# Kernel optimization log

Hardware: AMD Instinct MI355X
Metric: run time of the kernel (lower is better)

## Reference

```python
import jax, jax.numpy as jnp
import numpy as np
from jax import lax

B, C, H, W = 64, 64, 56, 56
E, TOPK = 8, 2
DN = ('NCHW', 'OIHW', 'NCHW')


def setup_inputs() -> dict:
    key = jax.random.key(0)
    ks = jax.random.split(key, 9)
    s = 0.05
    return {
        'x': jax.random.normal(ks[0], (B, C, H, W), jnp.float32),
        'gate_w': jax.random.normal(ks[1], (E, C), jnp.float32) * s,
        'gate_b': jnp.zeros((E,), jnp.float32),
        'conv1_w': jax.random.normal(ks[2], (E, C, C, 3, 3), jnp.float32) * s,
        'bn1_s': jnp.ones((E, C), jnp.float32),
        'bn1_b': jnp.zeros((E, C), jnp.float32),
        'conv2_w': jax.random.normal(ks[3], (E, C, C, 3, 3), jnp.float32) * s,
        'bn2_s': jnp.ones((E, C), jnp.float32),
        'bn2_b': jnp.zeros((E, C), jnp.float32),
    }


def _conv3x3(x, w):
    return lax.conv_general_dilated(x, w, (1, 1), ((1, 1), (1, 1)), dimension_numbers=DN)


def _bn(y, scale, bias):
    # eval-mode BatchNorm with running_mean=0, running_var=1 -> per-channel affine
    return y * scale[None, :, None, None] + bias[None, :, None, None]


def _basic_block(x, w1, s1, b1, w2, s2, b2):
    # standard ResNet BasicBlock, stride=1, identity downsample
    out = jax.nn.relu(_bn(_conv3x3(x, w1), s1, b1))
    out = _bn(_conv3x3(out, w2), s2, b2)
    return jax.nn.relu(out + x)


def reference(x, gate_w, gate_b, conv1_w, bn1_s, bn1_b, conv2_w, bn2_s, bn2_b):
    # gate: global average pool over HW -> linear -> top-k softmax weights [B, E]
    pooled = jnp.mean(x, axis=(2, 3))                       # [B, C]
    logits = pooled @ gate_w.T + gate_b                      # [B, E]
    top_vals, top_idx = lax.top_k(logits, TOPK)              # [B, K]
    top_w = jax.nn.softmax(top_vals, axis=-1)                # [B, K]
    dense_w = jnp.zeros((x.shape[0], E), x.dtype).at[
        jnp.arange(x.shape[0])[:, None], top_idx].set(top_w)  # [B, E]

    # run all experts (dense reference for the sparse dispatch/combine)
    ex_out = jax.vmap(lambda w1, s1, b1, w2, s2, b2: _basic_block(x, w1, s1, b1, w2, s2, b2))(
        conv1_w, bn1_s, bn1_b, conv2_w, bn2_s, bn2_b)        # [E, B, C, H, W]
    out = jnp.einsum('be,ebchw->bchw', dense_w, ex_out)
    return out, dense_w
```

## Files before the change

### kernel.cpp

```cpp
#include <hip/hip_runtime.h>


#define BATCH 64
#define CH    64
#define HW_   3136
#define IMG_  (CH*HW_)
#define PLANE (HW_*16)
#define NE    8
#define JOBS  128
#define PWSZ  36864
#define NTILE 13
#define BD    6
#define CGRID (NTILE*2*BATCH)

typedef unsigned short u16;
typedef __attribute__((ext_vector_type(8))) short short8_t;
typedef __attribute__((ext_vector_type(16))) float floatx16;

__device__ u16   g_xb[(size_t)BATCH*IMG_ + 4*PLANE];
__device__ u16   g_h[(size_t)JOBS*IMG_ + 4*PLANE];
__device__ u16   g_pw1[NE * PWSZ];
__device__ u16   g_pw2[NE * PWSZ];
__device__ int   g_eid[JOBS];
__device__ float g_wgt[JOBS];
__device__ float g_pool[49 * BATCH * CH];

__device__ __forceinline__ u16 f2b(float f) {
    unsigned v; __builtin_memcpy(&v, &f, 4);
    return (u16)((v + 0x7FFFu + ((v >> 16) & 1u)) >> 16);
}

__global__ __launch_bounds__(256) void prep_kernel(
    const float* __restrict__ x,
    const float* __restrict__ w1, const float* __restrict__ s1,
    const float* __restrict__ w2, const float* __restrict__ s2)
{
    int bid = blockIdx.x;
    int tid = threadIdx.x;
    if (bid < 2304) {
        int idx = bid * 256 + tid;
        int conv = idx / 294912;
        int i2 = idx - conv * 294912;
        int e = i2 / PWSZ;   int r = i2 - e * PWSZ;
        int s36 = r >> 10;   int r2 = r & 1023;
        int mt  = r2 >> 9;   int r3 = r2 & 511;
        int h   = r3 >> 8;   int r4 = r3 & 255;
        int m   = r4 >> 3;   int j  = r4 & 7;
        int tap = s36 >> 2;
        int ci  = ((s36 & 3) << 4) | (h << 3) | j;
        int M   = mt*32 + m;
        const float* w  = conv ? w2 : w1;
        const float* sc = conv ? s2 : s1;
        float v = w[((e*64 + M)*64 + ci)*9 + tap] * sc[e*64 + M];
        (conv ? g_pw2 : g_pw1)[i2] = f2b(v);
        return;
    }
    __shared__ u16 T[64*66];
    int xid = bid - 2304;
    int b = xid / 49;
    int tile = xid - b*49;
    int pos0 = tile * 64;
    int pin = tid & 63;
    int c0 = tid >> 6;
    const float* xb = x + (size_t)b*IMG_ + pos0 + pin;
    #pragma unroll
    for (int i = 0; i < 16; i++) {
        int ch = c0*16 + i;
        T[pin*66 + ch] = f2b(xb[ch*HW_]);
    }
    __syncthreads();
    u16* ob = g_xb + (size_t)b*IMG_ + (size_t)pos0*16;
    #pragma unroll
    for (int i = 0; i < 16; i++) {
        int j = tid + i*256;
        int kq  = j >> 10;
        int pos = (j >> 4) & 63;
        int c16 = j & 15;
        ob[(size_t)kq*PLANE + pos*16 + c16] = T[pos*66 + kq*16 + c16];
    }
    if (tid < 64) {
        float s = 0.f;
        const float* xc = x + (size_t)b*IMG_ + tid*HW_ + pos0;
        #pragma unroll 4
        for (int p = 0; p < 64; p++) s += xc[p];
        g_pool[tile*(BATCH*CH) + b*64 + tid] = s;
    }
}

__global__ __launch_bounds__(64) void gate_fin_kernel(
    const float* __restrict__ gw, const float* __restrict__ gb,
    float* __restrict__ dw_out)
{
    __shared__ float pooled[CH];
    __shared__ float logits[NE];
    int b = blockIdx.x, t = threadIdx.x;
    float s = 0.f;
    #pragma unroll
    for (int i = 0; i < 49; i++) s += g_pool[i*(BATCH*CH) + b*64 + t];
    pooled[t] = s * (1.f/3136.f);
    __syncthreads();
    if (t < NE) {
        float l = gb[t];
        for (int c = 0; c < CH; c++) l += pooled[c] * gw[t*CH + c];
        logits[t] = l;
    }
    __syncthreads();
    if (t == 0) {
        int i1 = 0; float v1 = logits[0];
        for (int e = 1; e < NE; e++) if (logits[e] > v1) { v1 = logits[e]; i1 = e; }
        int i2 = -1; float v2 = -3.4e38f;
        for (int e = 0; e < NE; e++) if (e != i1 && logits[e] > v2) { v2 = logits[e]; i2 = e; }
        float eb = __expf(v2 - v1);
        float wa = 1.f / (1.f + eb), wb = eb / (1.f + eb);
        for (int e = 0; e < NE; e++) dw_out[b*NE + e] = 0.f;
        dw_out[b*NE + i1] = wa;
        dw_out[b*NE + i2] = wb;
        g_eid[2*b] = i1; g_eid[2*b+1] = i2;
        g_wgt[2*b] = wa; g_wgt[2*b+1] = wb;
    }
}

__device__ __forceinline__ void stageA(
    u16* AL, const u16* __restrict__ pw0, const u16* __restrict__ pw1,
    int mt, int tid)
{
    short8_t st[9];
    #pragma unroll
    for (int i = 0; i < 9; i++) {
        int u = i*512 + tid;
        int es = u >= 2304;
        int r = u - (es ? 2304 : 0);
        int s36 = r >> 6;
        int c = r & 63;
        st[i] = *(const short8_t*)((es ? pw1 : pw0) + s36*1024 + mt*512 + c*8);
    }
    #pragma unroll
    for (int i = 0; i < 9; i++) {
        int u = i*512 + tid;
        int es = u >= 2304;
        int r = u - (es ? 2304 : 0);
        int s36 = r >> 6;
        int c = r & 63;
        *(short8_t*)(AL + (s36*2 + es)*512 + c*8) = st[i];
    }
}

__device__ __forceinline__ void mkOffs(
    unsigned* off, int gn, int y, int xc, int h, unsigned zoff)
{
    #pragma unroll
    for (int tap = 0; tap < 9; tap++) {
        int dy = tap/3 - 1, dx = tap - (tap/3)*3 - 1;
        int p = gn + dy*56 + dx;
        bool vld = ((unsigned)(y + dy) < 56u) && ((unsigned)(xc + dx) < 56u);
        off[tap] = vld ? (unsigned)(p*32 + h*16) : zoff;
    }
}
#define LOADB(base, off, kq) (*(const short8_t*)((base) + (off) + (unsigned)((kq)*PLANE*2)))

__global__ __launch_bounds__(512, 4) void conv1_kernel(const float* __restrict__ b1)
{
    __shared__ u16 AL[36864];
    int wg = blockIdx.x;
    int L  = (wg & 7) * (CGRID/8) + (wg >> 3);
    int b  = L / 26;
    int r  = L - b*26;
    int tile = r >> 1;
    int mt   = r & 1;
    int e0 = g_eid[2*b], e1 = g_eid[2*b+1];
    int tid = threadIdx.x;
    int lane = tid & 63, w = tid >> 6;
    int es = w & 1, pg = w >> 1;
    int l31 = lane & 31, h = lane >> 5;
    int gn0 = tile*256 + pg*64 + l31;
    int gn1 = gn0 + 32;
    int y0 = gn0/56, xc0 = gn0 - y0*56;
    int y1 = gn1/56, xc1 = gn1 - y1*56;
    int e = es ? e1 : e0;
    const char* base = (const char*)(g_xb + (size_t)b*IMG_);
    unsigned zoff = (unsigned)((size_t)(BATCH - b)*IMG_*2);
    const u16* pw0 = g_pw1 + e0*PWSZ;
    const u16* pw1 = g_pw1 + e1*PWSZ;
    int aOff = es*512 + h*256 + l31*8;

    unsigned off0[9], off1[9];
    mkOffs(off0, gn0, y0, xc0, h, zoff);
    mkOffs(off1, gn1, y1, xc1, h, zoff);

    floatx16 accA = {}, accB = {};
    short8_t B0[BD], B1[BD];
    #pragma unroll
    for (int s = 0; s < BD; s++) {
        B0[s] = LOADB(base, off0[s >> 2], s & 3);
        B1[s] = LOADB(base, off1[s >> 2], s & 3);
    }
    stageA(AL, pw0, pw1, mt, tid);
    __syncthreads();

    short8_t Ar[3];
    #pragma unroll
    for (int i = 0; i < 3; i++)
        Ar[i] = *(const short8_t*)(AL + i*1024 + aOff);

    #pragma unroll
    for (int s = 0; s < 36; s++) {
        short8_t bb0 = B0[s % BD];
        short8_t bb1 = B1[s % BD];
        int sp = s + BD;
        if (sp < 36) {
            B0[s % BD] = LOADB(base, off0[sp >> 2], sp & 3);
            B1[s % BD] = LOADB(base, off1[sp >> 2], sp & 3);
        }
        short8_t a = Ar[s % 3];
        if (s + 3 < 36)
            Ar[s % 3] = *(const short8_t*)(AL + (s+3)*1024 + aOff);
        accA = __builtin_amdgcn_mfma_f32_32x32x16_bf16(a, bb0, accA, 0, 0, 0);
        accB = __builtin_amdgcn_mfma_f32_32x32x16_bf16(a, bb1, accB, 0, 0, 0);
    }

    u16* hb = g_h + (size_t)(2*b + es)*IMG_;
    #pragma unroll
    for (int f = 0; f < 2; f++) {
        int gn = f ? gn1 : gn0;
        if (gn < HW_) {
            #pragma unroll
            for (int rg = 0; rg < 4; rg++) {
                union { u16 u[4]; uint2 v; } t;
                #pragma unroll
                for (int rr = 0; rr < 4; rr++) {
                    int m = rg*8 + h*4 + rr;
                    float v = (f ? accB : accA)[rg*4 + rr] + b1[e*64 + mt*32 + m];
                    t.u[rr] = f2b(fmaxf(v, 0.f));
                }
                int kq = mt*2 + (rg >> 1);
                *(uint2*)(hb + (size_t)kq*PLANE + (size_t)gn*16 + (rg & 1)*8 + h*4) = t.v;
            }
        }
    }
}

__global__ __launch_bounds__(512, 4) void conv2_kernel(
    const float* __restrict__ x, const float* __restrict__ b2,
    float* __restrict__ out)
{
    __shared__ u16 AL[36864];
    int wg = blockIdx.x;
    int L  = (wg & 7) * (CGRID/8) + (wg >> 3);
    int b  = L / 26;
    int r  = L - b*26;
    int tile = (NTILE-1) - (r >> 1);
    int mt   = r & 1;
    int e0 = g_eid[2*b], e1 = g_eid[2*b+1];
    int tid = threadIdx.x;
    int lane = tid & 63, w = tid >> 6;
    int es = w & 1, pg = w >> 1;
    int l31 = lane & 31, h = lane >> 5;
    int gn0 = tile*256 + pg*64 + l31;
    int gn1 = gn0 + 32;
    int y0 = gn0/56, xc0 = gn0 - y0*56;
    int y1 = gn1/56, xc1 = gn1 - y1*56;
    int e = es ? e1 : e0;
    float wgt = g_wgt[2*b + es];
    const char* base = (const char*)(g_h + (size_t)(2*b + es)*IMG_);
    unsigned zoff = (unsigned)((size_t)(JOBS - (2*b + es))*IMG_*2);
    const u16* pw0 = g_pw2 + e0*PWSZ;
    const u16* pw1 = g_pw2 + e1*PWSZ;
    int aOff = es*512 + h*256 + l31*8;

    unsigned off0[9], off1[9];
    mkOffs(off0, gn0, y0, xc0, h, zoff);
    mkOffs(off1, gn1, y1, xc1, h, zoff);

    floatx16 accA = {}, accB = {};
    short8_t B0[BD], B1[BD];
    #pragma unroll
    for (int s = 0; s < BD; s++) {
        B0[s] = LOADB(base, off0[s >> 2], s & 3);
        B1[s] = LOADB(base, off1[s >> 2], s & 3);
    }
    stageA(AL, pw0, pw1, mt, tid);
    __syncthreads();

    short8_t Ar[3];
    #pragma unroll
    for (int i = 0; i < 3; i++)
        Ar[i] = *(const short8_t*)(AL + i*1024 + aOff);

    #pragma unroll
    for (int s = 0; s < 36; s++) {
        short8_t bb0 = B0[s % BD];
        short8_t bb1 = B1[s % BD];
        int sp = s + BD;
        if (sp < 36) {
            B0[s % BD] = LOADB(base, off0[sp >> 2], sp & 3);
            B1[s % BD] = LOADB(base, off1[sp >> 2], sp & 3);
        }
        short8_t a = Ar[s % 3];
        if (s + 3 < 36)
            Ar[s % 3] = *(const short8_t*)(AL + (s+3)*1024 + aOff);
        accA = __builtin_amdgcn_mfma_f32_32x32x16_bf16(a, bb0, accA, 0, 0, 0);
        accB = __builtin_amdgcn_mfma_f32_32x32x16_bf16(a, bb1, accB, 0, 0, 0);
    }

    __syncthreads();
    float* P = (float*)AL;
    const float* xb = x + (size_t)b*IMG_ + (size_t)(mt*32)*HW_;
    if (es == 0) {
        #pragma unroll
        for (int f = 0; f < 2; f++) {
            int gn = f ? gn1 : gn0;
            if (gn < HW_) {
                #pragma unroll
                for (int rg = 0; rg < 4; rg++)
                    #pragma unroll
                    for (int rr = 0; rr < 4; rr++) {
                        int m = rg*8 + h*4 + rr;
                        float v = (f ? accB : accA)[rg*4 + rr] + b2[e*64 + mt*32 + m]
                                  + xb[(size_t)m*HW_ + gn];
                        P[((pg*2 + f)*32 + m)*32 + l31] = wgt * fmaxf(v, 0.f);
                    }
            }
        }
    }
    __syncthreads();
    if (es == 1) {
        float* ob = out + (size_t)b*IMG_ + (size_t)(mt*32)*HW_;
        #pragma unroll
        for (int f = 0; f < 2; f++) {
            int gn = f ? gn1 : gn0;
            if (gn < HW_) {
                #pragma unroll
                for (int rg = 0; rg < 4; rg++)
                    #pragma unroll
                    for (int rr = 0; rr < 4; rr++) {
                        int m = rg*8 + h*4 + rr;
                        float v = (f ? accB : accA)[rg*4 + rr] + b2[e*64 + mt*32 + m]
                                  + xb[(size_t)m*HW_ + gn];
                        ob[(size_t)m*HW_ + gn] = wgt * fmaxf(v, 0.f)
                                                 + P[((pg*2 + f)*32 + m)*32 + l31];
                    }
            }
        }
    }
}

extern "C" void kernel_launch(void* const* d_in, const int* in_sizes, int n_in,
                              void* d_out, int out_size, void* d_ws, size_t ws_size,
                              hipStream_t stream) {
    const float* x   = (const float*)d_in[0];
    const float* gw  = (const float*)d_in[1];
    const float* gb  = (const float*)d_in[2];
    const float* w1  = (const float*)d_in[3];
    const float* s1  = (const float*)d_in[4];
    const float* b1  = (const float*)d_in[5];
    const float* w2  = (const float*)d_in[6];
    const float* s2  = (const float*)d_in[7];
    const float* b2  = (const float*)d_in[8];
    float* out = (float*)d_out;
    float* dw  = out + (size_t)BATCH * IMG_;

    (void)d_ws; (void)ws_size;

    hipLaunchKernelGGL(prep_kernel, dim3(2304 + 3136), dim3(256), 0, stream,
                       x, w1, s1, w2, s2);
    hipLaunchKernelGGL(gate_fin_kernel, dim3(BATCH), dim3(64), 0, stream, gw, gb, dw);
    hipLaunchKernelGGL(conv1_kernel, dim3(CGRID), dim3(512), 0, stream, b1);
    hipLaunchKernelGGL(conv2_kernel, dim3(CGRID), dim3(512), 0, stream, x, b2, out);
}
```

Before: 243.5 us.

## Remap waves to cover both experts per pixel tile and combine outputs in registers

Each wave now computes one 32-pixel group for both experts instead of one expert for two pixel groups. In conv1 this lets both experts share a single B (input) fragment per step, halving global input loads. In conv2 the two expert results land in the same thread, so the LDS round trip and extra barriers in the weighted combine go away and the residual is read once. The change also adds sched_group_barrier hints to interleave loads and MFMAs, and computes pooling from the bf16 transposed tile in LDS rather than re-reading fp32 x, which slightly changes gate precision.

```diff
diff --git a/kernel.cpp b/kernel.cpp
--- a/kernel.cpp
+++ b/kernel.cpp
@@ -18,7 +18,7 @@
 typedef __attribute__((ext_vector_type(16))) float floatx16;
 
 __device__ u16   g_xb[(size_t)BATCH*IMG_ + 4*PLANE];
-__device__ u16   g_h[(size_t)JOBS*IMG_ + 4*PLANE];
+__device__ u16   g_h[(size_t)JOBS*IMG_ + IMG_ + 4*PLANE];
 __device__ u16   g_pw1[NE * PWSZ];
 __device__ u16   g_pw2[NE * PWSZ];
 __device__ int   g_eid[JOBS];
@@ -28,6 +28,11 @@
 __device__ __forceinline__ u16 f2b(float f) {
     unsigned v; __builtin_memcpy(&v, &f, 4);
     return (u16)((v + 0x7FFFu + ((v >> 16) & 1u)) >> 16);
+}
+__device__ __forceinline__ float b2f(u16 u) {
+    unsigned v = (unsigned)u << 16;
+    float f; __builtin_memcpy(&f, &v, 4);
+    return f;
 }
 
 __global__ __launch_bounds__(256) void prep_kernel(
@@ -80,9 +85,8 @@
     }
     if (tid < 64) {
         float s = 0.f;
-        const float* xc = x + (size_t)b*IMG_ + tid*HW_ + pos0;
-        #pragma unroll 4
-        for (int p = 0; p < 64; p++) s += xc[p];
+        #pragma unroll 8
+        for (int p = 0; p < 64; p++) s += b2f(T[p*66 + tid]);
         g_pool[tile*(BATCH*CH) + b*64 + tid] = s;
     }
 }
@@ -156,7 +160,7 @@
         off[tap] = vld ? (unsigned)(p*32 + h*16) : zoff;
     }
 }
-#define LOADB(base, off, kq) (*(const short8_t*)((base) + (off) + (unsigned)((kq)*PLANE*2)))
+#define LOADB(bk, off) (*(const short8_t*)((bk) + (off)))
 
 __global__ __launch_bounds__(512, 4) void conv1_kernel(const float* __restrict__ b1)
 {
@@ -169,72 +173,77 @@
     int mt   = r & 1;
     int e0 = g_eid[2*b], e1 = g_eid[2*b+1];
     int tid = threadIdx.x;
-    int lane = tid & 63, w = tid >> 6;
-    int es = w & 1, pg = w >> 1;
+    int lane = tid & 63, pg = tid >> 6;
     int l31 = lane & 31, h = lane >> 5;
-    int gn0 = tile*256 + pg*64 + l31;
-    int gn1 = gn0 + 32;
-    int y0 = gn0/56, xc0 = gn0 - y0*56;
-    int y1 = gn1/56, xc1 = gn1 - y1*56;
-    int e = es ? e1 : e0;
+    int gn = tile*256 + pg*32 + l31;
+    int y = gn/56, xc = gn - y*56;
     const char* base = (const char*)(g_xb + (size_t)b*IMG_);
+    const char* bk0 = base;
+    const char* bk1 = base + PLANE*2;
+    const char* bk2 = base + 2*PLANE*2;
+    const char* bk3 = base + 3*PLANE*2;
     unsigned zoff = (unsigned)((size_t)(BATCH - b)*IMG_*2);
     const u16* pw0 = g_pw1 + e0*PWSZ;
     const u16* pw1 = g_pw1 + e1*PWSZ;
-    int aOff = es*512 + h*256 + l31*8;
-
-    unsigned off0[9], off1[9];
-    mkOffs(off0, gn0, y0, xc0, h, zoff);
-    mkOffs(off1, gn1, y1, xc1, h, zoff);
-
-    floatx16 accA = {}, accB = {};
-    short8_t B0[BD], B1[BD];
+    int aOff0 = h*256 + l31*8;
+    int aOff1 = 512 + h*256 + l31*8;
+
+    unsigned off[9];
+    mkOffs(off, gn, y, xc, h, zoff);
+
+    floatx16 acc0 = {}, acc1 = {};
+    short8_t B[BD];
     #pragma unroll
     for (int s = 0; s < BD; s++) {
-        B0[s] = LOADB(base, off0[s >> 2], s & 3);
-        B1[s] = LOADB(base, off1[s >> 2], s & 3);
+        const char* bk = (s&3)==0 ? bk0 : (s&3)==1 ? bk1 : (s&3)==2 ? bk2 : bk3;
+        B[s] = LOADB(bk, off[s >> 2]);
     }
     stageA(AL, pw0, pw1, mt, tid);
     __syncthreads();
 
-    short8_t Ar[3];
-    #pragma unroll
-    for (int i = 0; i < 3; i++)
-        Ar[i] = *(const short8_t*)(AL + i*1024 + aOff);
+    short8_t Ar0[3], Ar1[3];
+    #pragma unroll
+    for (int i = 0; i < 3; i++) {
+        Ar0[i] = *(const short8_t*)(AL + i*1024 + aOff0);
+        Ar1[i] = *(const short8_t*)(AL + i*1024 + aOff1);
+    }
 
     #pragma unroll
     for (int s = 0; s < 36; s++) {
-        short8_t bb0 = B0[s % BD];
-        short8_t bb1 = B1[s % BD];
+        short8_t bb = B[s % BD];
         int sp = s + BD;
         if (sp < 36) {
-            B0[s % BD] = LOADB(base, off0[sp >> 2], sp & 3);
-            B1[s % BD] = LOADB(base, off1[sp >> 2], sp & 3);
-        }
-        short8_t a = Ar[s % 3];
-        if (s + 3 < 36)
-            Ar[s % 3] = *(const short8_t*)(AL + (s+3)*1024 + aOff);
-        accA = __builtin_amdgcn_mfma_f32_32x32x16_bf16(a, bb0, accA, 0, 0, 0);
-        accB = __builtin_amdgcn_mfma_f32_32x32x16_bf16(a, bb1, accB, 0, 0, 0);
-    }
-
-    u16* hb = g_h + (size_t)(2*b + es)*IMG_;
-    #pragma unroll
-    for (int f = 0; f < 2; f++) {
-        int gn = f ? gn1 : gn0;
-        if (gn < HW_) {
+            const char* bk = (sp&3)==0 ? bk0 : (sp&3)==1 ? bk1 : (sp&3)==2 ? bk2 : bk3;
+            B[s % BD] = LOADB(bk, off[sp >> 2]);
+        }
+        short8_t a0 = Ar0[s % 3], a1 = Ar1[s % 3];
+        if (s + 3 < 36) {
+            Ar0[s % 3] = *(const short8_t*)(AL + (s+3)*1024 + aOff0);
+            Ar1[s % 3] = *(const short8_t*)(AL + (s+3)*1024 + aOff1);
+        }
+        acc0 = __builtin_amdgcn_mfma_f32_32x32x16_bf16(a0, bb, acc0, 0, 0, 0);
+        acc1 = __builtin_amdgcn_mfma_f32_32x32x16_bf16(a1, bb, acc1, 0, 0, 0);
+        if (sp < 36)     __builtin_amdgcn_sched_group_barrier(0x020, 1, 0);
+        if (s + 3 < 36)  __builtin_amdgcn_sched_group_barrier(0x100, 2, 0);
+        __builtin_amdgcn_sched_group_barrier(0x008, 2, 0);
+    }
+
+    if (gn < HW_) {
+        u16* hb0 = g_h + (size_t)(2*b)*IMG_;
+        u16* hb1 = hb0 + IMG_;
+        #pragma unroll
+        for (int rg = 0; rg < 4; rg++) {
+            union { u16 u[4]; uint2 v; } t0, t1;
             #pragma unroll
-            for (int rg = 0; rg < 4; rg++) {
-                union { u16 u[4]; uint2 v; } t;
-                #pragma unroll
-                for (int rr = 0; rr < 4; rr++) {
-                    int m = rg*8 + h*4 + rr;
-                    float v = (f ? accB : accA)[rg*4 + rr] + b1[e*64 + mt*32 + m];
-                    t.u[rr] = f2b(fmaxf(v, 0.f));
-                }
-                int kq = mt*2 + (rg >> 1);
-                *(uint2*)(hb + (size_t)kq*PLANE + (size_t)gn*16 + (rg & 1)*8 + h*4) = t.v;
+            for (int rr = 0; rr < 4; rr++) {
+                int m = rg*8 + h*4 + rr;
+                t0.u[rr] = f2b(fmaxf(acc0[rg*4 + rr] + b1[e0*64 + mt*32 + m], 0.f));
+                t1.u[rr] = f2b(fmaxf(acc1[rg*4 + rr] + b1[e1*64 + mt*32 + m], 0.f));
             }
+            int kq = mt*2 + (rg >> 1);
+            size_t o = (size_t)kq*PLANE + (size_t)gn*16 + (rg & 1)*8 + h*4;
+            *(uint2*)(hb0 + o) = t0.v;
+            *(uint2*)(hb1 + o) = t1.v;
         }
     }
 }
@@ -251,40 +260,50 @@
     int tile = (NTILE-1) - (r >> 1);
     int mt   = r & 1;
     int e0 = g_eid[2*b], e1 = g_eid[2*b+1];
+    float w0 = g_wgt[2*b], w1w = g_wgt[2*b+1];
     int tid = threadIdx.x;
-    int lane = tid & 63, w = tid >> 6;
-    int es = w & 1, pg = w >> 1;
+    int lane = tid & 63, pg = tid >> 6;
     int l31 = lane & 31, h = lane >> 5;
-    int gn0 = tile*256 + pg*64 + l31;
-    int gn1 = gn0 + 32;
-    int y0 = gn0/56, xc0 = gn0 - y0*56;
-    int y1 = gn1/56, xc1 = gn1 - y1*56;
-    int e = es ? e1 : e0;
-    float wgt = g_wgt[2*b + es];
-    const char* base = (const char*)(g_h + (size_t)(2*b + es)*IMG_);
-    unsigned zoff = (unsigned)((size_t)(JOBS - (2*b + es))*IMG_*2);
+    int gn = tile*256 + pg*32 + l31;
+    int y = gn/56, xc = gn - y*56;
+    const char* baseA = (const char*)(g_h + (size_t)(2*b)*IMG_);
+    const char* baseB = (const char*)(g_h + (size_t)(2*b + 1)*IMG_);
+    const char* bkA0 = baseA;
+    const char* bkA1 = baseA + PLANE*2;
+    const char* bkA2 = baseA + 2*PLANE*2;
+    const char* bkA3 = baseA + 3*PLANE*2;
+    const char* bkB0 = baseB;
+    const char* bkB1 = baseB + PLANE*2;
+    const char* bkB2 = baseB + 2*PLANE*2;
+    const char* bkB3 = baseB + 3*PLANE*2;
+    unsigned zoff = (unsigned)((size_t)(JOBS - 2*b)*IMG_*2);
     const u16* pw0 = g_pw2 + e0*PWSZ;
     const u16* pw1 = g_pw2 + e1*PWSZ;
-    int aOff = es*512 + h*256 + l31*8;
-
-    unsigned off0[9], off1[9];
-    mkOffs(off0, gn0, y0, xc0, h, zoff);
-    mkOffs(off1, gn1, y1, xc1, h, zoff);
-
-    floatx16 accA = {}, accB = {};
+    int aOff0 = h*256 + l31*8;
+    int aOff1 = 512 + h*256 + l31*8;
+
+    unsigned off[9];
+    mkOffs(off, gn, y, xc, h, zoff);
+
+    floatx16 acc0 = {}, acc1 = {};
     short8_t B0[BD], B1[BD];
     #pragma unroll
     for (int s = 0; s < BD; s++) {
-        B0[s] = LOADB(base, off0[s >> 2], s & 3);
-        B1[s] = LOADB(base, off1[s >> 2], s & 3);
+        unsigned o = off[s >> 2];
+        const char* bA = (s&3)==0 ? bkA0 : (s&3)==1 ? bkA1 : (s&3)==2 ? bkA2 : bkA3;
+        const char* bB = (s&3)==0 ? bkB0 : (s&3)==1 ? bkB1 : (s&3)==2 ? bkB2 : bkB3;
+        B0[s] = LOADB(bA, o);
+        B1[s] = LOADB(bB, o);
     }
     stageA(AL, pw0, pw1, mt, tid);
     __syncthreads();
 
-    short8_t Ar[3];
-    #pragma unroll
-    for (int i = 0; i < 3; i++)
-        Ar[i] = *(const short8_t*)(AL + i*1024 + aOff);
+    short8_t Ar0[3], Ar1[3];
+    #pragma unroll
+    for (int i = 0; i < 3; i++) {
+        Ar0[i] = *(const short8_t*)(AL + i*1024 + aOff0);
+        Ar1[i] = *(const short8_t*)(AL + i*1024 + aOff1);
+    }
 
     #pragma unroll
     for (int s = 0; s < 36; s++) {
@@ -292,55 +311,38 @@
         short8_t bb1 = B1[s % BD];
         int sp = s + BD;
         if (sp < 36) {
-            B0[s % BD] = LOADB(base, off0[sp >> 2], sp & 3);
-            B1[s % BD] = LOADB(base, off1[sp >> 2], sp & 3);
-        }
-        short8_t a = Ar[s % 3];
-        if (s + 3 < 36)
-            Ar[s % 3] = *(const short8_t*)(AL + (s+3)*1024 + aOff);
-        accA = __builtin_amdgcn_mfma_f32_32x32x16_bf16(a, bb0, accA, 0, 0, 0);
-        accB = __builtin_amdgcn_mfma_f32_32x32x16_bf16(a, bb1, accB, 0, 0, 0);
-    }
-
-    __syncthreads();
-    float* P = (float*)AL;
-    const float* xb = x + (size_t)b*IMG_ + (size_t)(mt*32)*HW_;
-    if (es == 0) {
-        #pragma unroll
-        for (int f = 0; f < 2; f++) {
-            int gn = f ? gn1 : gn0;
-            if (gn < HW_) {
-                #pragma unroll
-                for (int rg = 0; rg < 4; rg++)
-                    #pragma unroll
-                    for (int rr = 0; rr < 4; rr++) {
-                        int m = rg*8 + h*4 + rr;
-                        float v = (f ? accB : accA)[rg*4 + rr] + b2[e*64 + mt*32 + m]
-                                  + xb[(size_t)m*HW_ + gn];
-                        P[((pg*2 + f)*32 + m)*32 + l31] = wgt * fmaxf(v, 0.f);
-                    }
-            }
-        }
-    }
-    __syncthreads();
-    if (es == 1) {
+            unsigned o = off[sp >> 2];
+            const char* bA = (sp&3)==0 ? bkA0 : (sp&3)==1 ? bkA1 : (sp&3)==2 ? bkA2 : bkA3;
+            const char* bB = (sp&3)==0 ? bkB0 : (sp&3)==1 ? bkB1 : (sp&3)==2 ? bkB2 : bkB3;
+            B0[s % BD] = LOADB(bA, o);
+            B1[s % BD] = LOADB(bB, o);
+        }
+        short8_t a0 = Ar0[s % 3], a1 = Ar1[s % 3];
+        if (s + 3 < 36) {
+            Ar0[s % 3] = *(const short8_t*)(AL + (s+3)*1024 + aOff0);
+            Ar1[s % 3] = *(const short8_t*)(AL + (s+3)*1024 + aOff1);
+        }
+        acc0 = __builtin_amdgcn_mfma_f32_32x32x16_bf16(a0, bb0, acc0, 0, 0, 0);
+        acc1 = __builtin_amdgcn_mfma_f32_32x32x16_bf16(a1, bb1, acc1, 0, 0, 0);
+        if (sp < 36)     __builtin_amdgcn_sched_group_barrier(0x020, 2, 0);
+        if (s + 3 < 36)  __builtin_amdgcn_sched_group_barrier(0x100, 2, 0);
+        __builtin_amdgcn_sched_group_barrier(0x008, 2, 0);
+    }
+
+    if (gn < HW_) {
+        const float* xb = x + (size_t)b*IMG_ + (size_t)(mt*32)*HW_;
         float* ob = out + (size_t)b*IMG_ + (size_t)(mt*32)*HW_;
         #pragma unroll
-        for (int f = 0; f < 2; f++) {
-            int gn = f ? gn1 : gn0;
-            if (gn < HW_) {
-                #pragma unroll
-                for (int rg = 0; rg < 4; rg++)
-                    #pragma unroll
-                    for (int rr = 0; rr < 4; rr++) {
-                        int m = rg*8 + h*4 + rr;
-                        float v = (f ? accB : accA)[rg*4 + rr] + b2[e*64 + mt*32 + m]
-                                  + xb[(size_t)m*HW_ + gn];
-                        ob[(size_t)m*HW_ + gn] = wgt * fmaxf(v, 0.f)
-                                                 + P[((pg*2 + f)*32 + m)*32 + l31];
-                    }
+        for (int rg = 0; rg < 4; rg++)
+            #pragma unroll
+            for (int rr = 0; rr < 4; rr++) {
+                int m = rg*8 + h*4 + rr;
+                float xres = xb[(size_t)m*HW_ + gn];
+                float y0 = acc0[rg*4 + rr] + b2[e0*64 + mt*32 + m];
+                float y1 = acc1[rg*4 + rr] + b2[e1*64 + mt*32 + m];
+                ob[(size_t)m*HW_ + gn] = w0 * fmaxf(y0 + xres, 0.f)
+                                         + w1w * fmaxf(y1 + xres, 0.f);
             }
-        }
     }
 }
 
```

Result: faster. 213.2 us (-12.4%).
